# Kernel optimization log

Hardware: AMD Instinct MI355X
Metric: run time of the kernel (lower is better)

Reference implementation:

```python
import jax, jax.numpy as jnp
import numpy as np

N_NODES = 50000
N_EDGES = 800000
IN_DIM = 128
EDGE_DIM = 16
HIDDEN = 128
N_LAYERS = 3
N_GRAPHS = 256
BN_EPS = 1e-5


def setup_inputs() -> dict:
    key = jax.random.key(0)
    ks = jax.random.split(key, 24)
    s = 0.05
    inp = {
        "x": jax.random.normal(ks[0], (N_NODES, IN_DIM), jnp.float32),
        "edge_index": jax.random.randint(ks[1], (2, N_EDGES), 0, N_NODES, jnp.int32),
        "edge_attr": jax.random.normal(ks[2], (N_EDGES, EDGE_DIM), jnp.float32),
        "batch": jnp.sort(jax.random.randint(ks[3], (N_NODES,), 0, N_GRAPHS, jnp.int32)),
        "n_graphs": N_GRAPHS,
        # input projection
        "lin_in_w": jax.random.normal(ks[4], (IN_DIM, HIDDEN), jnp.float32) * s,
        "lin_in_b": jnp.zeros((HIDDEN,), jnp.float32),
        # per-layer message MLP (stacked over layers)
        "msg_w1": jax.random.normal(ks[5], (N_LAYERS, HIDDEN + EDGE_DIM, HIDDEN), jnp.float32) * s,
        "msg_b1": jnp.zeros((N_LAYERS, HIDDEN), jnp.float32),
        "msg_w2": jax.random.normal(ks[6], (N_LAYERS, HIDDEN, HIDDEN), jnp.float32) * s,
        "msg_b2": jnp.zeros((N_LAYERS, HIDDEN), jnp.float32),
        # BatchNorm (eval mode: running stats)
        "bn_gamma": jnp.ones((N_LAYERS, HIDDEN), jnp.float32),
        "bn_beta": jnp.zeros((N_LAYERS, HIDDEN), jnp.float32),
        "bn_mean": jax.random.normal(ks[7], (N_LAYERS, HIDDEN), jnp.float32) * 0.01,
        "bn_var": jax.random.uniform(ks[8], (N_LAYERS, HIDDEN), jnp.float32, 0.5, 1.5),
        # GRUCell params (PyTorch layout: [3*H, H], gate order r,z,n)
        "gru_wih": jax.random.normal(ks[9], (N_LAYERS, 3 * HIDDEN, HIDDEN), jnp.float32) * s,
        "gru_whh": jax.random.normal(ks[10], (N_LAYERS, 3 * HIDDEN, HIDDEN), jnp.float32) * s,
        "gru_bih": jnp.zeros((N_LAYERS, 3 * HIDDEN), jnp.float32),
        "gru_bhh": jnp.zeros((N_LAYERS, 3 * HIDDEN), jnp.float32),
        # readout linear: [2H -> H]
        "ro_w": jax.random.normal(ks[11], (2 * HIDDEN, HIDDEN), jnp.float32) * s,
        "ro_b": jnp.zeros((HIDDEN,), jnp.float32),
    }
    return inp


def _gru_cell(x, h, wih, whh, bih, bhh):
    gi = x @ wih.T + bih  # [N, 3H]
    gh = h @ whh.T + bhh
    ir, iz, inn = jnp.split(gi, 3, axis=1)
    hr, hz, hn = jnp.split(gh, 3, axis=1)
    r = jax.nn.sigmoid(ir + hr)
    z = jax.nn.sigmoid(iz + hz)
    n = jnp.tanh(inn + r * hn)
    return (1.0 - z) * n + z * h


def reference(x, edge_index, edge_attr, batch, n_graphs,
              lin_in_w, lin_in_b, msg_w1, msg_b1, msg_w2, msg_b2,
              bn_gamma, bn_beta, bn_mean, bn_var,
              gru_wih, gru_whh, gru_bih, gru_bhh, ro_w, ro_b):
    h = jax.nn.relu(x @ lin_in_w + lin_in_b)  # [N, H]
    src, dst = edge_index[0], edge_index[1]
    n_nodes = h.shape[0]
    for l in range(N_LAYERS):
        m_in = jnp.concatenate([h[src], edge_attr], axis=1)  # [E, H+Ed]
        m = jax.nn.relu(m_in @ msg_w1[l] + msg_b1[l]) @ msg_w2[l] + msg_b2[l]  # [E, H]
        agg = jax.ops.segment_sum(m, dst, num_segments=n_nodes)  # scatter-add
        h_new = _gru_cell(agg, h, gru_wih[l], gru_whh[l], gru_bih[l], gru_bhh[l])
        bn = (h_new - bn_mean[l]) * jax.lax.rsqrt(bn_var[l] + BN_EPS) * bn_gamma[l] + bn_beta[l]
        h = h + bn  # dropout is identity in eval mode
    # readout: segment mean + segment max over graphs
    cnt = jax.ops.segment_sum(jnp.ones((n_nodes, 1), h.dtype), batch, num_segments=n_graphs)
    z_sum = jax.ops.segment_sum(h, batch, num_segments=n_graphs)
    z_mean = z_sum / jnp.maximum(cnt, 1.0)
    z_max = jax.ops.segment_max(h, batch, num_segments=n_graphs)
    z_max = jnp.where(cnt > 0, z_max, 0.0)  # empty graphs -> 0 (as in torch code)
    z = jax.nn.relu(jnp.concatenate([z_mean, z_max], axis=1) @ ro_w + ro_b)
    return z
```

## Files before the change

kernel.cpp:

```cpp
#include <hip/hip_runtime.h>
#include <math.h>

constexpr int NN = 50000;
constexpr int NE = 800000;
constexpr int H  = 128;
constexpr int ED = 16;
constexpr int NL = 3;
constexpr int NG = 256;

typedef __attribute__((ext_vector_type(8))) short bf8;
typedef __attribute__((ext_vector_type(4))) float f32x4;

__device__ __forceinline__ unsigned short f2bf(float f) {
    unsigned u = __float_as_uint(f);
    unsigned r = (u + 0x7FFFu + ((u >> 16) & 1u)) >> 16;
    return (unsigned short)r;
}
__device__ __forceinline__ float bf2f(unsigned short b) {
    return __uint_as_float(((unsigned)b) << 16);
}

__global__ __launch_bounds__(256) void k_zero4(float4* __restrict__ a, int n4) {
    int i = blockIdx.x * 256 + threadIdx.x;
    if (i < n4) a[i] = make_float4(0.f, 0.f, 0.f, 0.f);
}

__global__ __launch_bounds__(256) void k_sort_zero(int* __restrict__ counts) {
    int i = blockIdx.x * 256 + threadIdx.x;
    counts[i] = 0;
}

__global__ __launch_bounds__(256) void k_hist(const int* __restrict__ ei,
                                              int* __restrict__ counts) {
    int e = blockIdx.x * 256 + threadIdx.x;
    if (e < NE) atomicAdd(&counts[ei[NE + e]], 1);
}

__global__ __launch_bounds__(256) void k_scan1(const int* __restrict__ counts,
                                               int* __restrict__ incl,
                                               int* __restrict__ bsum) {
    __shared__ int s[256];
    int t = threadIdx.x;
    int i = blockIdx.x * 256 + t;
    int v = counts[i];
    s[t] = v;
    __syncthreads();
    #pragma unroll
    for (int off = 1; off < 256; off <<= 1) {
        int x = (t >= off) ? s[t - off] : 0;
        __syncthreads();
        s[t] += x;
        __syncthreads();
    }
    incl[i] = s[t];
    if (t == 255) bsum[blockIdx.x] = s[255];
}

__global__ __launch_bounds__(256) void k_scan2(int* __restrict__ bsum) {
    __shared__ int s[256];
    int t = threadIdx.x;
    int v = (t < 196) ? bsum[t] : 0;
    s[t] = v;
    __syncthreads();
    #pragma unroll
    for (int off = 1; off < 256; off <<= 1) {
        int x = (t >= off) ? s[t - off] : 0;
        __syncthreads();
        s[t] += x;
        __syncthreads();
    }
    if (t < 196) bsum[t] = s[t] - v;
}

__global__ __launch_bounds__(256) void k_scan3(const int* __restrict__ counts,
                                               const int* __restrict__ incl,
                                               const int* __restrict__ bsum,
                                               int* __restrict__ cur) {
    int i = blockIdx.x * 256 + threadIdx.x;
    cur[i] = incl[i] - counts[i] + bsum[blockIdx.x];
}

__global__ __launch_bounds__(256) void k_scatter_perm(const int* __restrict__ ei,
                                                      int* __restrict__ cur,
                                                      int* __restrict__ perm) {
    int e = blockIdx.x * 256 + threadIdx.x;
    if (e < NE) {
        int d = ei[NE + e];
        int pos = atomicAdd(&cur[d], 1);
        perm[pos] = e;
    }
}

__global__ __launch_bounds__(256) void k_gather(const int* __restrict__ ei,
                                                const float* __restrict__ ea,
                                                int* __restrict__ perm,
                                                int* __restrict__ dsts,
                                                unsigned short* __restrict__ ea_bf) {
    int i = blockIdx.x * 256 + threadIdx.x;
    if (i >= NE) return;
    int e = perm[i];
    perm[i] = ei[e];
    dsts[i] = ei[NE + e];
    const float4* s = (const float4*)(ea + (size_t)e * ED);
    float4 v[4];
    #pragma unroll
    for (int j = 0; j < 4; ++j) v[j] = s[j];
    union { uint4 u[2]; unsigned short sh[16]; } pk;
    #pragma unroll
    for (int j = 0; j < 4; ++j) {
        pk.sh[j * 4 + 0] = f2bf(v[j].x); pk.sh[j * 4 + 1] = f2bf(v[j].y);
        pk.sh[j * 4 + 2] = f2bf(v[j].z); pk.sh[j * 4 + 3] = f2bf(v[j].w);
    }
    uint4* d = (uint4*)(ea_bf + (size_t)i * 16);
    d[0] = pk.u[0];
    d[1] = pk.u[1];
}

__global__ __launch_bounds__(256) void k_prep(const float* __restrict__ wih,
                                              const float* __restrict__ whh,
                                              const float* __restrict__ w1,
                                              const float* __restrict__ w2,
                                              const float* __restrict__ lin_w,
                                              unsigned short* __restrict__ wgru,
                                              unsigned short* __restrict__ w1et,
                                              unsigned short* __restrict__ w2t,
                                              unsigned short* __restrict__ w1ht,
                                              unsigned short* __restrict__ winT) {
    int i = blockIdx.x * 256 + threadIdx.x;
    if (i < 294912) {
        int m = i / 147456, rem = i % 147456;
        wgru[i] = f2bf((m == 0 ? wih : whh)[rem]);
        return;
    }
    i -= 294912;
    if (i < NL * 128 * 32) {
        int l = i / 4096, rem = i % 4096;
        int n = rem >> 5, k = rem & 31;
        float v = (k < ED) ? w1[(size_t)l * 144 * 128 + (size_t)(128 + k) * 128 + n] : 0.f;
        w1et[i] = f2bf(v);
        return;
    }
    i -= NL * 128 * 32;
    if (i < NL * 128 * 128) {
        int l = i / 16384, rem = i % 16384;
        int n = rem >> 7, k = rem & 127;
        w2t[i] = f2bf(w2[(size_t)l * 16384 + (size_t)k * 128 + n]);
        return;
    }
    i -= NL * 128 * 128;
    if (i < NL * 128 * 128) {
        int l = i / 16384, rem = i % 16384;
        int n = rem >> 7, k = rem & 127;
        w1ht[i] = f2bf(w1[(size_t)l * 144 * 128 + (size_t)k * 128 + n]);
        return;
    }
    i -= NL * 128 * 128;
    if (i < 128 * 128) {
        int n = i >> 7, k = i & 127;
        winT[i] = f2bf(lin_w[k * 128 + n]);
    }
}

__global__ __launch_bounds__(256) void k_inproj(const float* __restrict__ x,
                                                const unsigned short* __restrict__ winT,
                                                const float* __restrict__ bias,
                                                const unsigned short* __restrict__ w1h0,
                                                float* __restrict__ h,
                                                unsigned short* __restrict__ p_bf) {
    __shared__ unsigned short As[32][136];
    const int t = threadIdx.x;
    const int w = t >> 6, lane = t & 63, l15 = lane & 15, q = lane >> 4;
    const int n0 = blockIdx.x * 32;

    bf8 bfr[2][4];
    #pragma unroll
    for (int nt = 0; nt < 2; ++nt) {
        int n = w * 32 + nt * 16 + l15;
        #pragma unroll
        for (int ks = 0; ks < 4; ++ks)
            bfr[nt][ks] = *(const bf8*)(winT + (size_t)n * 128 + ks * 32 + q * 8);
    }

    {
        int r = t >> 3, cs = (t & 7) * 16;
        int row = n0 + r;
        float4 v[4];
        if (row < NN) {
            const float4* src = (const float4*)(x + (size_t)row * H + cs);
            #pragma unroll
            for (int j = 0; j < 4; ++j) v[j] = src[j];
        } else {
            #pragma unroll
            for (int j = 0; j < 4; ++j) v[j] = make_float4(0.f, 0.f, 0.f, 0.f);
        }
        union { uint4 u[2]; unsigned short s[16]; } pk;
        #pragma unroll
        for (int j = 0; j < 4; ++j) {
            pk.s[j * 4 + 0] = f2bf(v[j].x); pk.s[j * 4 + 1] = f2bf(v[j].y);
            pk.s[j * 4 + 2] = f2bf(v[j].z); pk.s[j * 4 + 3] = f2bf(v[j].w);
        }
        *(uint4*)&As[r][cs] = pk.u[0];
        *(uint4*)&As[r][cs + 8] = pk.u[1];
    }
    __syncthreads();

    f32x4 acc[2][2];
    #pragma unroll
    for (int mt = 0; mt < 2; ++mt)
        #pragma unroll
        for (int nt = 0; nt < 2; ++nt) acc[mt][nt] = {0.f, 0.f, 0.f, 0.f};

    #pragma unroll
    for (int ks = 0; ks < 4; ++ks) {
        #pragma unroll
        for (int mt = 0; mt < 2; ++mt) {
            bf8 af = *(const bf8*)&As[mt * 16 + l15][ks * 32 + q * 8];
            acc[mt][0] = __builtin_amdgcn_mfma_f32_16x16x32_bf16(af, bfr[0][ks], acc[mt][0], 0, 0, 0);
            acc[mt][1] = __builtin_amdgcn_mfma_f32_16x16x32_bf16(af, bfr[1][ks], acc[mt][1], 0, 0, 0);
        }
    }
    __syncthreads();

    #pragma unroll
    for (int nt = 0; nt < 2; ++nt) {
        int col = w * 32 + nt * 16 + l15;
        float bv = bias[col];
        #pragma unroll
        for (int mt = 0; mt < 2; ++mt) {
            #pragma unroll
            for (int r = 0; r < 4; ++r) {
                int nl = mt * 16 + q * 4 + r;
                int node = n0 + nl;
                float v = fmaxf(acc[mt][nt][r] + bv, 0.f);
                if (node < NN) h[(size_t)node * H + col] = v;
                As[nl][col] = f2bf(v);
            }
        }
    }
    __syncthreads();

    bf8 pfr[2][4];
    #pragma unroll
    for (int nt = 0; nt < 2; ++nt) {
        int n = w * 32 + nt * 16 + l15;
        #pragma unroll
        for (int ks = 0; ks < 4; ++ks)
            pfr[nt][ks] = *(const bf8*)(w1h0 + (size_t)n * 128 + ks * 32 + q * 8);
    }
    f32x4 accp[2][2];
    #pragma unroll
    for (int mt = 0; mt < 2; ++mt)
        #pragma unroll
        for (int nt = 0; nt < 2; ++nt) accp[mt][nt] = {0.f, 0.f, 0.f, 0.f};
    #pragma unroll
    for (int ks = 0; ks < 4; ++ks) {
        #pragma unroll
        for (int mt = 0; mt < 2; ++mt) {
            bf8 af = *(const bf8*)&As[mt * 16 + l15][ks * 32 + q * 8];
            accp[mt][0] = __builtin_amdgcn_mfma_f32_16x16x32_bf16(af, pfr[0][ks], accp[mt][0], 0, 0, 0);
            accp[mt][1] = __builtin_amdgcn_mfma_f32_16x16x32_bf16(af, pfr[1][ks], accp[mt][1], 0, 0, 0);
        }
    }
    #pragma unroll
    for (int nt = 0; nt < 2; ++nt) {
        int col = w * 32 + nt * 16 + l15;
        #pragma unroll
        for (int mt = 0; mt < 2; ++mt) {
            #pragma unroll
            for (int r = 0; r < 4; ++r) {
                int node = n0 + mt * 16 + q * 4 + r;
                if (node < NN) p_bf[(size_t)node * H + col] = f2bf(accp[mt][nt][r]);
            }
        }
    }
}

__global__ __launch_bounds__(256, 4) void k_edge_mfma(
        const unsigned short* __restrict__ p,
        const int* __restrict__ srcs,
        const int* __restrict__ dsts,
        const unsigned short* __restrict__ ea_bf,
        const unsigned short* __restrict__ w1et,
        const float* __restrict__ b1,
        const unsigned short* __restrict__ w2t,
        const float* __restrict__ b2,
        float* __restrict__ agg) {
    __shared__ unsigned short u_s[64][136];
    __shared__ int src_s[64], dst_s[64];

    const int t    = threadIdx.x;
    const int w    = t >> 6;
    const int lane = t & 63;
    const int l15  = lane & 15;
    const int q    = lane >> 4;

    bf8 w1f[2];
    bf8 w2f[2][4];
    float b1v[2], b2v[2];
    #pragma unroll
    for (int nt = 0; nt < 2; ++nt) {
        int n = w * 32 + nt * 16 + l15;
        w1f[nt] = *(const bf8*)(w1et + (size_t)n * 32 + q * 8);
        #pragma unroll
        for (int ks = 0; ks < 4; ++ks)
            w2f[nt][ks] = *(const bf8*)(w2t + (size_t)n * 128 + ks * 32 + q * 8);
        b1v[nt] = b1[n];
        b2v[nt] = b2[n];
    }

    const f32x4 zero = {0.f, 0.f, 0.f, 0.f};

    for (int base = blockIdx.x * 64; base < NE; base += gridDim.x * 64) {
        if (t < 64)       src_s[t] = srcs[base + t];
        else if (t < 128) dst_s[t - 64] = dsts[base + t - 64];
        __syncthreads();

        {
            int row = t >> 4, seg = t & 15;
            #pragma unroll
            for (int it = 0; it < 4; ++it) {
                int rr = row + 16 * it;
                *(uint4*)&u_s[rr][seg * 8] =
                    *(const uint4*)(p + (size_t)src_s[rr] * H + seg * 8);
            }
        }

        f32x4 acc1[4][2];
        #pragma unroll
        for (int mt = 0; mt < 4; ++mt) {
            bf8 af = {0, 0, 0, 0, 0, 0, 0, 0};
            if (q < 2)
                af = *(const bf8*)(ea_bf + (size_t)(base + mt * 16 + l15) * 16 + q * 8);
            #pragma unroll
            for (int nt = 0; nt < 2; ++nt)
                acc1[mt][nt] = __builtin_amdgcn_mfma_f32_16x16x32_bf16(af, w1f[nt], zero, 0, 0, 0);
        }
        __syncthreads();

        #pragma unroll
        for (int mt = 0; mt < 4; ++mt) {
            #pragma unroll
            for (int r = 0; r < 4; ++r) {
                int er = mt * 16 + q * 4 + r;
                #pragma unroll
                for (int nt = 0; nt < 2; ++nt) {
                    int col = w * 32 + nt * 16 + l15;
                    float v = acc1[mt][nt][r] + bf2f(u_s[er][col]) + b1v[nt];
                    u_s[er][col] = f2bf(fmaxf(v, 0.f));
                }
            }
        }
        __syncthreads();

        f32x4 acc2[4][2];
        #pragma unroll
        for (int mt = 0; mt < 4; ++mt)
            #pragma unroll
            for (int nt = 0; nt < 2; ++nt) acc2[mt][nt] = zero;

        #pragma unroll
        for (int ks = 0; ks < 4; ++ks) {
            #pragma unroll
            for (int mt = 0; mt < 4; ++mt) {
                bf8 af = *(const bf8*)&u_s[mt * 16 + l15][ks * 32 + q * 8];
                acc2[mt][0] = __builtin_amdgcn_mfma_f32_16x16x32_bf16(af, w2f[0][ks], acc2[mt][0], 0, 0, 0);
                acc2[mt][1] = __builtin_amdgcn_mfma_f32_16x16x32_bf16(af, w2f[1][ks], acc2[mt][1], 0, 0, 0);
            }
        }
        __syncthreads();

        #pragma unroll
        for (int mt = 0; mt < 4; ++mt) {
            #pragma unroll
            for (int r = 0; r < 4; ++r) {
                int er = mt * 16 + q * 4 + r;
                #pragma unroll
                for (int nt = 0; nt < 2; ++nt) {
                    int col = w * 32 + nt * 16 + l15;
                    u_s[er][col] = f2bf(acc2[mt][nt][r] + b2v[nt]);
                }
            }
        }
        __syncthreads();

        {
            int c = t & 127, hh = t >> 7;
            float sum = 0.f;
            int prev = dst_s[hh * 32];
            #pragma unroll 4
            for (int i = 0; i < 32; ++i) {
                int e = hh * 32 + i;
                int d = dst_s[e];
                float v = bf2f(u_s[e][c]);
                if (d != prev) {
                    atomicAdd(&agg[(size_t)prev * H + c], sum);
                    sum = 0.f;
                    prev = d;
                }
                sum += v;
            }
            atomicAdd(&agg[(size_t)prev * H + c], sum);
        }
        __syncthreads();
    }
}

__device__ __forceinline__ float sigmoidf_(float x) { return 1.f / (1.f + expf(-x)); }

__global__ __launch_bounds__(256) void k_gru_mfma(const float* __restrict__ agg,
                                                  float* __restrict__ h,
                                                  const unsigned short* __restrict__ wih,
                                                  const unsigned short* __restrict__ whh,
                                                  const float* __restrict__ bih,
                                                  const float* __restrict__ bhh,
                                                  const float* __restrict__ gamma,
                                                  const float* __restrict__ beta,
                                                  const float* __restrict__ mean,
                                                  const float* __restrict__ var,
                                                  const unsigned short* __restrict__ w1h_next,
                                                  unsigned short* __restrict__ p_bf) {
    __shared__ unsigned short ab[32][136];
    __shared__ unsigned short hb[32][136];
    __shared__ float hf[32][132];
    const int t = threadIdx.x;
    const int w = t >> 6, lane = t & 63, l15 = lane & 15, q = lane >> 4;
    const int n0 = blockIdx.x * 32;

    {
        int r = t >> 3, cs = (t & 7) * 16;
        int row = n0 + r;
        float4 va[4], vh[4];
        if (row < NN) {
            const float4* sa = (const float4*)(agg + (size_t)row * H + cs);
            const float4* sh = (const float4*)(h + (size_t)row * H + cs);
            #pragma unroll
            for (int j = 0; j < 4; ++j) { va[j] = sa[j]; vh[j] = sh[j]; }
        } else {
            #pragma unroll
            for (int j = 0; j < 4; ++j) {
                va[j] = make_float4(0.f, 0.f, 0.f, 0.f);
                vh[j] = va[j];
            }
        }
        union { uint4 u[2]; unsigned short s[16]; } pa, ph;
        #pragma unroll
        for (int j = 0; j < 4; ++j) {
            pa.s[j * 4 + 0] = f2bf(va[j].x); pa.s[j * 4 + 1] = f2bf(va[j].y);
            pa.s[j * 4 + 2] = f2bf(va[j].z); pa.s[j * 4 + 3] = f2bf(va[j].w);
            ph.s[j * 4 + 0] = f2bf(vh[j].x); ph.s[j * 4 + 1] = f2bf(vh[j].y);
            ph.s[j * 4 + 2] = f2bf(vh[j].z); ph.s[j * 4 + 3] = f2bf(vh[j].w);
            *(float4*)&hf[r][cs + j * 4] = vh[j];
        }
        *(uint4*)&ab[r][cs] = pa.u[0];  *(uint4*)&ab[r][cs + 8] = pa.u[1];
        *(uint4*)&hb[r][cs] = ph.u[0];  *(uint4*)&hb[r][cs + 8] = ph.u[1];
    }
    __syncthreads();

    f32x4 acc[2][2][3][2];
    #pragma unroll
    for (int mt = 0; mt < 2; ++mt)
        #pragma unroll
        for (int io = 0; io < 2; ++io)
            #pragma unroll
            for (int g = 0; g < 3; ++g)
                #pragma unroll
                for (int nt = 0; nt < 2; ++nt) acc[mt][io][g][nt] = {0.f, 0.f, 0.f, 0.f};

    #pragma unroll
    for (int ks = 0; ks < 4; ++ks) {
        bf8 a_a[2], a_h[2];
        #pragma unroll
        for (int mt = 0; mt < 2; ++mt) {
            a_a[mt] = *(const bf8*)&ab[mt * 16 + l15][ks * 32 + q * 8];
            a_h[mt] = *(const bf8*)&hb[mt * 16 + l15][ks * 32 + q * 8];
        }
        #pragma unroll
        for (int g = 0; g < 3; ++g) {
            #pragma unroll
            for (int nt = 0; nt < 2; ++nt) {
                int n = g * 128 + w * 32 + nt * 16 + l15;
                bf8 bi = *(const bf8*)(wih + (size_t)n * 128 + ks * 32 + q * 8);
                bf8 bh = *(const bf8*)(whh + (size_t)n * 128 + ks * 32 + q * 8);
                #pragma unroll
                for (int mt = 0; mt < 2; ++mt) {
                    acc[mt][0][g][nt] = __builtin_amdgcn_mfma_f32_16x16x32_bf16(a_a[mt], bi, acc[mt][0][g][nt], 0, 0, 0);
                    acc[mt][1][g][nt] = __builtin_amdgcn_mfma_f32_16x16x32_bf16(a_h[mt], bh, acc[mt][1][g][nt], 0, 0, 0);
                }
            }
        }
    }

    float rout[2][2][4];
    #pragma unroll
    for (int nt = 0; nt < 2; ++nt) {
        int col = w * 32 + nt * 16 + l15;
        float bir = bih[col], biz = bih[128 + col], bin = bih[256 + col];
        float bhr = bhh[col], bhz = bhh[128 + col], bhn = bhh[256 + col];
        float ga = gamma[col], be = beta[col], mu = mean[col];
        float iv = rsqrtf(var[col] + 1e-5f);
        #pragma unroll
        for (int mt = 0; mt < 2; ++mt) {
            #pragma unroll
            for (int r = 0; r < 4; ++r) {
                int nl = mt * 16 + q * 4 + r;
                int node = n0 + nl;
                float ir = acc[mt][0][0][nt][r] + bir;
                float iz = acc[mt][0][1][nt][r] + biz;
                float in = acc[mt][0][2][nt][r] + bin;
                float hr = acc[mt][1][0][nt][r] + bhr;
                float hz = acc[mt][1][1][nt][r] + bhz;
                float hn = acc[mt][1][2][nt][r] + bhn;
                float rg = sigmoidf_(ir + hr);
                float zg = sigmoidf_(iz + hz);
                float ng = tanhf(in + rg * hn);
                float hv = hf[nl][col];
                float hnew = (1.f - zg) * ng + zg * hv;
                float bn = (hnew - mu) * iv * ga + be;
                float out = hv + bn;
                rout[nt][mt][r] = out;
                if (node < NN) h[(size_t)node * H + col] = out;
            }
        }
    }

    if (w1h_next != nullptr) {
        __syncthreads();
        #pragma unroll
        for (int nt = 0; nt < 2; ++nt) {
            int col = w * 32 + nt * 16 + l15;
            #pragma unroll
            for (int mt = 0; mt < 2; ++mt)
                #pragma unroll
                for (int r = 0; r < 4; ++r)
                    hb[mt * 16 + q * 4 + r][col] = f2bf(rout[nt][mt][r]);
        }
        __syncthreads();

        f32x4 accp[2][2];
        #pragma unroll
        for (int mt = 0; mt < 2; ++mt)
            #pragma unroll
            for (int nt = 0; nt < 2; ++nt) accp[mt][nt] = {0.f, 0.f, 0.f, 0.f};
        #pragma unroll
        for (int ks = 0; ks < 4; ++ks) {
            bf8 pf0, pf1;
            {
                int n = w * 32 + l15;
                pf0 = *(const bf8*)(w1h_next + (size_t)n * 128 + ks * 32 + q * 8);
                pf1 = *(const bf8*)(w1h_next + (size_t)(n + 16) * 128 + ks * 32 + q * 8);
            }
            #pragma unroll
            for (int mt = 0; mt < 2; ++mt) {
                bf8 af = *(const bf8*)&hb[mt * 16 + l15][ks * 32 + q * 8];
                accp[mt][0] = __builtin_amdgcn_mfma_f32_16x16x32_bf16(af, pf0, accp[mt][0], 0, 0, 0);
                accp[mt][1] = __builtin_amdgcn_mfma_f32_16x16x32_bf16(af, pf1, accp[mt][1], 0, 0, 0);
            }
        }
        #pragma unroll
        for (int nt = 0; nt < 2; ++nt) {
            int col = w * 32 + nt * 16 + l15;
            #pragma unroll
            for (int mt = 0; mt < 2; ++mt) {
                #pragma unroll
                for (int r = 0; r < 4; ++r) {
                    int node = n0 + mt * 16 + q * 4 + r;
                    if (node < NN) p_bf[(size_t)node * H + col] = f2bf(accp[mt][nt][r]);
                }
            }
        }
    }
}

__device__ __forceinline__ unsigned fkey(float f) {
    unsigned b = __float_as_uint(f);
    return (b & 0x80000000u) ? ~b : (b | 0x80000000u);
}
__device__ __forceinline__ float funkey(unsigned k) {
    unsigned b = (k & 0x80000000u) ? (k & 0x7FFFFFFFu) : ~k;
    return __uint_as_float(b);
}

__global__ __launch_bounds__(256) void k_ro_init(float* __restrict__ gsum,
                                                 unsigned* __restrict__ gmaxb,
                                                 float* __restrict__ gcnt) {
    int i = blockIdx.x * 256 + threadIdx.x;
    if (i < NG * H) { gsum[i] = 0.f; gmaxb[i] = 0u; }
    if (i < NG) gcnt[i] = 0.f;
}

__global__ __launch_bounds__(256) void k_ro_scan(const float* __restrict__ h,
                                                 const int* __restrict__ batch,
                                                 float* __restrict__ gsum,
                                                 unsigned* __restrict__ gmaxb,
                                                 float* __restrict__ gcnt) {
    __shared__ int bt_s[64];
    const int t = threadIdx.x;
    const int n0 = blockIdx.x * 64;
    if (t < 64) bt_s[t] = (n0 + t < NN) ? batch[n0 + t] : -1;
    __syncthreads();

    int c = t & 127, hh = t >> 7;
    float sum = 0.f, mx = -3.4e38f, cnt = 0.f;
    int prev = bt_s[hh * 32];
    #pragma unroll 4
    for (int i = 0; i < 32; ++i) {
        int e = hh * 32 + i;
        int g = bt_s[e];
        if (g != prev) {
            if (prev >= 0) {
                atomicAdd(&gsum[prev * H + c], sum);
                atomicMax(&gmaxb[prev * H + c], fkey(mx));
                if (c == 0) atomicAdd(&gcnt[prev], cnt);
            }
            sum = 0.f; mx = -3.4e38f; cnt = 0.f;
            prev = g;
        }
        if (g >= 0) {
            float v = h[(size_t)(n0 + e) * H + c];
            sum += v;
            mx = fmaxf(mx, v);
            cnt += 1.f;
        }
    }
    if (prev >= 0) {
        atomicAdd(&gsum[prev * H + c], sum);
        atomicMax(&gmaxb[prev * H + c], fkey(mx));
        if (c == 0) atomicAdd(&gcnt[prev], cnt);
    }
}

__global__ __launch_bounds__(128) void k_ro_final(const float* __restrict__ gsum,
                                                  const unsigned* __restrict__ gmaxb,
                                                  const float* __restrict__ gcnt,
                                                  const float* __restrict__ row,
                                                  const float* __restrict__ rob,
                                                  float* __restrict__ out) {
    __shared__ float cat[256];
    const int g = blockIdx.x, t = threadIdx.x;
    float cnt = gcnt[g];
    float inv = 1.f / fmaxf(cnt, 1.f);
    cat[t] = gsum[g * H + t] * inv;
    float mx = funkey(gmaxb[g * H + t]);
    cat[128 + t] = (cnt > 0.f) ? mx : 0.f;
    __syncthreads();
    float acc = rob[t];
    #pragma unroll 4
    for (int k = 0; k < 256; ++k) acc += cat[k] * row[k * H + t];
    out[g * H + t] = fmaxf(acc, 0.f);
}

extern "C" void kernel_launch(void* const* d_in, const int* in_sizes, int n_in,
                              void* d_out, int out_size, void* d_ws, size_t ws_size,
                              hipStream_t stream) {
    const float* x        = (const float*)d_in[0];
    const int*   ei       = (const int*)d_in[1];
    const float* ea       = (const float*)d_in[2];
    const int*   batch    = (const int*)d_in[3];
    const float* lin_in_w = (const float*)d_in[5];
    const float* lin_in_b = (const float*)d_in[6];
    const float* msg_w1   = (const float*)d_in[7];
    const float* msg_b1   = (const float*)d_in[8];
    const float* msg_w2   = (const float*)d_in[9];
    const float* msg_b2   = (const float*)d_in[10];
    const float* bn_gamma = (const float*)d_in[11];
    const float* bn_beta  = (const float*)d_in[12];
    const float* bn_mean  = (const float*)d_in[13];
    const float* bn_var   = (const float*)d_in[14];
    const float* gru_wih  = (const float*)d_in[15];
    const float* gru_whh  = (const float*)d_in[16];
    const float* gru_bih  = (const float*)d_in[17];
    const float* gru_bhh  = (const float*)d_in[18];
    const float* ro_w     = (const float*)d_in[19];
    const float* ro_b     = (const float*)d_in[20];

    float* ws = (float*)d_ws;
    float*          h     = ws;
    float*          agg   = ws + 6400000;
    unsigned short* p_bf  = (unsigned short*)(ws + 12800000);
    float*          gsum  = ws + 16000000;
    unsigned*       gmaxb = (unsigned*)(ws + 16032768);
    float*          gcnt  = ws + 16065536;
    unsigned short* wgru  = (unsigned short*)(ws + 16065792);
    unsigned short* w1et  = (unsigned short*)(ws + 16213248);
    unsigned short* w2t   = (unsigned short*)(ws + 16219392);
    unsigned short* w1ht  = (unsigned short*)(ws + 16243968);
    unsigned short* winT  = (unsigned short*)(ws + 16268544);
    int*            cnts  = (int*)(ws + 16276736);
    int*            incl  = (int*)(ws + 16326912);
    int*            cur   = (int*)(ws + 16377088);
    int*            bsum  = (int*)(ws + 16427264);
    int*            srcs  = (int*)(ws + 16427520);
    int*            dsts  = (int*)(ws + 17227520);
    unsigned short* ea_bf = (unsigned short*)(ws + 18027520);

    k_prep<<<1648, 256, 0, stream>>>(gru_wih, gru_whh, msg_w1, msg_w2, lin_in_w,
                                     wgru, w1et, w2t, w1ht, winT);

    k_sort_zero<<<196, 256, 0, stream>>>(cnts);
    k_hist<<<3125, 256, 0, stream>>>(ei, cnts);
    k_scan1<<<196, 256, 0, stream>>>(cnts, incl, bsum);
    k_scan2<<<1, 256, 0, stream>>>(bsum);
    k_scan3<<<196, 256, 0, stream>>>(cnts, incl, bsum, cur);
    k_scatter_perm<<<3125, 256, 0, stream>>>(ei, cur, srcs);
    k_gather<<<3125, 256, 0, stream>>>(ei, ea, srcs, dsts, ea_bf);

    k_inproj<<<1563, 256, 0, stream>>>(x, winT, lin_in_b, w1ht, h, p_bf);

    for (int l = 0; l < NL; ++l) {
        k_zero4<<<6250, 256, 0, stream>>>((float4*)agg, 1600000);
        k_edge_mfma<<<1024, 256, 0, stream>>>(p_bf, srcs, dsts, ea_bf,
                                              w1et + (size_t)l * 4096, msg_b1 + l * 128,
                                              w2t + (size_t)l * 16384, msg_b2 + l * 128,
                                              agg);
        const unsigned short* w1h_next = (l + 1 < NL) ? (w1ht + (size_t)(l + 1) * 16384) : nullptr;
        k_gru_mfma<<<1563, 256, 0, stream>>>(agg, h,
                                             wgru + (size_t)l * 49152,
                                             wgru + (size_t)(NL + l) * 49152,
                                             gru_bih + l * 384, gru_bhh + l * 384,
                                             bn_gamma + l * 128, bn_beta + l * 128,
                                             bn_mean + l * 128, bn_var + l * 128,
                                             w1h_next, p_bf);
    }

    k_ro_init<<<128, 256, 0, stream>>>(gsum, gmaxb, gcnt);
    k_ro_scan<<<782, 256, 0, stream>>>(h, batch, gsum, gmaxb, gcnt);
    k_ro_final<<<NG, 128, 0, stream>>>(gsum, gmaxb, gcnt, ro_w, ro_b, (float*)d_out);
}
```

Before: 849.6 us.

## Fuse preprocessing into cooperative kernel, fold zeroing into compute kernels, enlarge edge tile

Replaces the chain of preprocessing kernels (weight prep, histogram, three scans, permutation scatter, gather) with a single cooperative kernel that uses grid-wide syncs. The separate agg and readout zeroing kernels are removed: agg is zeroed inside the input projection and GRU kernels, and the readout accumulators are zeroed in the last GRU launch. The edge kernel tile grows from 64 to 128 edges, processed in two halves, and the GRU activations switch to fast exp-based sigmoid and tanh. The aim is fewer launches and less zeroing traffic. The trade-offs are grid-sync overhead, a 256-block cooperative grid doing strided work, more shared memory per edge block, and slightly different numerics.

```diff
diff --git a/kernel.cpp b/kernel.cpp
--- a/kernel.cpp
+++ b/kernel.cpp
@@ -1,5 +1,8 @@
 #include <hip/hip_runtime.h>
+#include <hip/hip_cooperative_groups.h>
 #include <math.h>
+
+namespace cg = cooperative_groups;
 
 constexpr int NN = 50000;
 constexpr int NE = 800000;
@@ -7,6 +10,9 @@
 constexpr int ED = 16;
 constexpr int NL = 3;
 constexpr int NG = 256;
+constexpr int NBINS = 50176;
+constexpr int TE = 128;
+constexpr int PREP_TOTAL = 294912 + NL*128*32 + NL*128*128 + NL*128*128 + 128*128;
 
 typedef __attribute__((ext_vector_type(8))) short bf8;
 typedef __attribute__((ext_vector_type(4))) float f32x4;
@@ -19,114 +25,22 @@
 __device__ __forceinline__ float bf2f(unsigned short b) {
     return __uint_as_float(((unsigned)b) << 16);
 }
-
-__global__ __launch_bounds__(256) void k_zero4(float4* __restrict__ a, int n4) {
-    int i = blockIdx.x * 256 + threadIdx.x;
-    if (i < n4) a[i] = make_float4(0.f, 0.f, 0.f, 0.f);
-}
-
-__global__ __launch_bounds__(256) void k_sort_zero(int* __restrict__ counts) {
-    int i = blockIdx.x * 256 + threadIdx.x;
-    counts[i] = 0;
-}
-
-__global__ __launch_bounds__(256) void k_hist(const int* __restrict__ ei,
-                                              int* __restrict__ counts) {
-    int e = blockIdx.x * 256 + threadIdx.x;
-    if (e < NE) atomicAdd(&counts[ei[NE + e]], 1);
-}
-
-__global__ __launch_bounds__(256) void k_scan1(const int* __restrict__ counts,
-                                               int* __restrict__ incl,
-                                               int* __restrict__ bsum) {
-    __shared__ int s[256];
-    int t = threadIdx.x;
-    int i = blockIdx.x * 256 + t;
-    int v = counts[i];
-    s[t] = v;
-    __syncthreads();
-    #pragma unroll
-    for (int off = 1; off < 256; off <<= 1) {
-        int x = (t >= off) ? s[t - off] : 0;
-        __syncthreads();
-        s[t] += x;
-        __syncthreads();
-    }
-    incl[i] = s[t];
-    if (t == 255) bsum[blockIdx.x] = s[255];
-}
-
-__global__ __launch_bounds__(256) void k_scan2(int* __restrict__ bsum) {
-    __shared__ int s[256];
-    int t = threadIdx.x;
-    int v = (t < 196) ? bsum[t] : 0;
-    s[t] = v;
-    __syncthreads();
-    #pragma unroll
-    for (int off = 1; off < 256; off <<= 1) {
-        int x = (t >= off) ? s[t - off] : 0;
-        __syncthreads();
-        s[t] += x;
-        __syncthreads();
-    }
-    if (t < 196) bsum[t] = s[t] - v;
-}
-
-__global__ __launch_bounds__(256) void k_scan3(const int* __restrict__ counts,
-                                               const int* __restrict__ incl,
-                                               const int* __restrict__ bsum,
-                                               int* __restrict__ cur) {
-    int i = blockIdx.x * 256 + threadIdx.x;
-    cur[i] = incl[i] - counts[i] + bsum[blockIdx.x];
-}
-
-__global__ __launch_bounds__(256) void k_scatter_perm(const int* __restrict__ ei,
-                                                      int* __restrict__ cur,
-                                                      int* __restrict__ perm) {
-    int e = blockIdx.x * 256 + threadIdx.x;
-    if (e < NE) {
-        int d = ei[NE + e];
-        int pos = atomicAdd(&cur[d], 1);
-        perm[pos] = e;
-    }
-}
-
-__global__ __launch_bounds__(256) void k_gather(const int* __restrict__ ei,
-                                                const float* __restrict__ ea,
-                                                int* __restrict__ perm,
-                                                int* __restrict__ dsts,
-                                                unsigned short* __restrict__ ea_bf) {
-    int i = blockIdx.x * 256 + threadIdx.x;
-    if (i >= NE) return;
-    int e = perm[i];
-    perm[i] = ei[e];
-    dsts[i] = ei[NE + e];
-    const float4* s = (const float4*)(ea + (size_t)e * ED);
-    float4 v[4];
-    #pragma unroll
-    for (int j = 0; j < 4; ++j) v[j] = s[j];
-    union { uint4 u[2]; unsigned short sh[16]; } pk;
-    #pragma unroll
-    for (int j = 0; j < 4; ++j) {
-        pk.sh[j * 4 + 0] = f2bf(v[j].x); pk.sh[j * 4 + 1] = f2bf(v[j].y);
-        pk.sh[j * 4 + 2] = f2bf(v[j].z); pk.sh[j * 4 + 3] = f2bf(v[j].w);
-    }
-    uint4* d = (uint4*)(ea_bf + (size_t)i * 16);
-    d[0] = pk.u[0];
-    d[1] = pk.u[1];
-}
-
-__global__ __launch_bounds__(256) void k_prep(const float* __restrict__ wih,
-                                              const float* __restrict__ whh,
-                                              const float* __restrict__ w1,
-                                              const float* __restrict__ w2,
-                                              const float* __restrict__ lin_w,
-                                              unsigned short* __restrict__ wgru,
-                                              unsigned short* __restrict__ w1et,
-                                              unsigned short* __restrict__ w2t,
-                                              unsigned short* __restrict__ w1ht,
-                                              unsigned short* __restrict__ winT) {
-    int i = blockIdx.x * 256 + threadIdx.x;
+__device__ __forceinline__ float fsig(float x) {
+    float e = __expf(fminf(-x, 80.f));
+    return 1.f / (1.f + e);
+}
+__device__ __forceinline__ float ftanh_(float x) {
+    float e = __expf(fminf(-2.f * x, 80.f));
+    return (1.f - e) / (1.f + e);
+}
+
+__device__ __forceinline__ void prep_one(int i,
+        const float* __restrict__ wih, const float* __restrict__ whh,
+        const float* __restrict__ w1, const float* __restrict__ w2,
+        const float* __restrict__ lin_w,
+        unsigned short* __restrict__ wgru, unsigned short* __restrict__ w1et,
+        unsigned short* __restrict__ w2t, unsigned short* __restrict__ w1ht,
+        unsigned short* __restrict__ winT) {
     if (i < 294912) {
         int m = i / 147456, rem = i % 147456;
         wgru[i] = f2bf((m == 0 ? wih : whh)[rem]);
@@ -161,12 +75,96 @@
     }
 }
 
+__global__ __launch_bounds__(256) void k_coop(
+        const float* __restrict__ wih, const float* __restrict__ whh,
+        const float* __restrict__ w1, const float* __restrict__ w2,
+        const float* __restrict__ lin_w,
+        unsigned short* __restrict__ wgru, unsigned short* __restrict__ w1et,
+        unsigned short* __restrict__ w2t, unsigned short* __restrict__ w1ht,
+        unsigned short* __restrict__ winT,
+        const int* __restrict__ ei, const float* __restrict__ ea,
+        int* __restrict__ cnts, int* __restrict__ incl, int* __restrict__ bsum,
+        int* __restrict__ cur, int* __restrict__ srcs, int* __restrict__ dsts,
+        unsigned short* __restrict__ ea_bf) {
+    cg::grid_group grid = cg::this_grid();
+    const int t = threadIdx.x;
+    const int gid = blockIdx.x * 256 + t;
+    const int GT = gridDim.x * 256;
+    __shared__ int s[256];
+
+    if (gid < NBINS) cnts[gid] = 0;
+    for (int i = gid; i < PREP_TOTAL; i += GT)
+        prep_one(i, wih, whh, w1, w2, lin_w, wgru, w1et, w2t, w1ht, winT);
+    grid.sync();
+
+    for (int e = gid; e < NE; e += GT) atomicAdd(&cnts[ei[NE + e]], 1);
+    grid.sync();
+
+    if (blockIdx.x < 196) {
+        int v = cnts[gid];
+        s[t] = v;
+        __syncthreads();
+        #pragma unroll
+        for (int off = 1; off < 256; off <<= 1) {
+            int x2 = (t >= off) ? s[t - off] : 0;
+            __syncthreads();
+            s[t] += x2;
+            __syncthreads();
+        }
+        incl[gid] = s[t];
+        if (t == 255) bsum[blockIdx.x] = s[255];
+    }
+    grid.sync();
+
+    if (blockIdx.x == 0) {
+        int v = (t < 196) ? bsum[t] : 0;
+        s[t] = v;
+        __syncthreads();
+        #pragma unroll
+        for (int off = 1; off < 256; off <<= 1) {
+            int x2 = (t >= off) ? s[t - off] : 0;
+            __syncthreads();
+            s[t] += x2;
+            __syncthreads();
+        }
+        if (t < 196) bsum[t] = s[t] - v;
+    }
+    grid.sync();
+
+    if (gid < NBINS) cur[gid] = incl[gid] - cnts[gid] + bsum[gid >> 8];
+    grid.sync();
+
+    for (int e = gid; e < NE; e += GT) {
+        int d = ei[NE + e];
+        int pos = atomicAdd(&cur[d], 1);
+        srcs[pos] = e;
+    }
+    grid.sync();
+
+    for (int i = gid; i < NE; i += GT) {
+        int e = srcs[i];
+        srcs[i] = ei[e];
+        dsts[i] = ei[NE + e];
+        const float4* sp = (const float4*)(ea + (size_t)e * ED);
+        float4 v0 = sp[0], v1 = sp[1], v2 = sp[2], v3 = sp[3];
+        union { uint4 u[2]; unsigned short sh[16]; } pk;
+        pk.sh[0] = f2bf(v0.x); pk.sh[1] = f2bf(v0.y); pk.sh[2] = f2bf(v0.z); pk.sh[3] = f2bf(v0.w);
+        pk.sh[4] = f2bf(v1.x); pk.sh[5] = f2bf(v1.y); pk.sh[6] = f2bf(v1.z); pk.sh[7] = f2bf(v1.w);
+        pk.sh[8] = f2bf(v2.x); pk.sh[9] = f2bf(v2.y); pk.sh[10] = f2bf(v2.z); pk.sh[11] = f2bf(v2.w);
+        pk.sh[12] = f2bf(v3.x); pk.sh[13] = f2bf(v3.y); pk.sh[14] = f2bf(v3.z); pk.sh[15] = f2bf(v3.w);
+        uint4* d4 = (uint4*)(ea_bf + (size_t)i * 16);
+        d4[0] = pk.u[0];
+        d4[1] = pk.u[1];
+    }
+}
+
 __global__ __launch_bounds__(256) void k_inproj(const float* __restrict__ x,
                                                 const unsigned short* __restrict__ winT,
                                                 const float* __restrict__ bias,
                                                 const unsigned short* __restrict__ w1h0,
                                                 float* __restrict__ h,
-                                                unsigned short* __restrict__ p_bf) {
+                                                unsigned short* __restrict__ p_bf,
+                                                float* __restrict__ agg) {
     __shared__ unsigned short As[32][136];
     const int t = threadIdx.x;
     const int w = t >> 6, lane = t & 63, l15 = lane & 15, q = lane >> 4;
@@ -203,6 +201,16 @@
         *(uint4*)&As[r][cs + 8] = pk.u[1];
     }
     __syncthreads();
+
+    {
+        int r = t >> 3, cs = (t & 7) * 16;
+        int row = n0 + r;
+        if (row < NN) {
+            float4 z = make_float4(0.f, 0.f, 0.f, 0.f);
+            float4* dz = (float4*)(agg + (size_t)row * H + cs);
+            dz[0] = z; dz[1] = z; dz[2] = z; dz[3] = z;
+        }
+    }
 
     f32x4 acc[2][2];
     #pragma unroll
@@ -285,8 +293,8 @@
         const unsigned short* __restrict__ w2t,
         const float* __restrict__ b2,
         float* __restrict__ agg) {
-    __shared__ unsigned short u_s[64][136];
-    __shared__ int src_s[64], dst_s[64];
+    __shared__ unsigned short u_s[TE][136];
+    __shared__ int src_s[TE], dst_s[TE];
 
     const int t    = threadIdx.x;
     const int w    = t >> 6;
@@ -310,74 +318,78 @@
 
     const f32x4 zero = {0.f, 0.f, 0.f, 0.f};
 
-    for (int base = blockIdx.x * 64; base < NE; base += gridDim.x * 64) {
-        if (t < 64)       src_s[t] = srcs[base + t];
-        else if (t < 128) dst_s[t - 64] = dsts[base + t - 64];
+    for (int base = blockIdx.x * TE; base < NE; base += gridDim.x * TE) {
+        if (t < TE) src_s[t] = srcs[base + t];
+        else        dst_s[t - TE] = dsts[base + t - TE];
         __syncthreads();
 
         {
             int row = t >> 4, seg = t & 15;
             #pragma unroll
-            for (int it = 0; it < 4; ++it) {
+            for (int it = 0; it < 8; ++it) {
                 int rr = row + 16 * it;
                 *(uint4*)&u_s[rr][seg * 8] =
                     *(const uint4*)(p + (size_t)src_s[rr] * H + seg * 8);
             }
         }
 
-        f32x4 acc1[4][2];
-        #pragma unroll
-        for (int mt = 0; mt < 4; ++mt) {
-            bf8 af = {0, 0, 0, 0, 0, 0, 0, 0};
-            if (q < 2)
-                af = *(const bf8*)(ea_bf + (size_t)(base + mt * 16 + l15) * 16 + q * 8);
-            #pragma unroll
-            for (int nt = 0; nt < 2; ++nt)
-                acc1[mt][nt] = __builtin_amdgcn_mfma_f32_16x16x32_bf16(af, w1f[nt], zero, 0, 0, 0);
+        #pragma unroll
+        for (int half = 0; half < 2; ++half) {
+            f32x4 acc1[4][2];
+            #pragma unroll
+            for (int m4 = 0; m4 < 4; ++m4) {
+                int mt = half * 4 + m4;
+                bf8 af = {0, 0, 0, 0, 0, 0, 0, 0};
+                if (q < 2)
+                    af = *(const bf8*)(ea_bf + (size_t)(base + mt * 16 + l15) * 16 + q * 8);
+                acc1[m4][0] = __builtin_amdgcn_mfma_f32_16x16x32_bf16(af, w1f[0], zero, 0, 0, 0);
+                acc1[m4][1] = __builtin_amdgcn_mfma_f32_16x16x32_bf16(af, w1f[1], zero, 0, 0, 0);
+            }
+            if (half == 0) __syncthreads();
+            #pragma unroll
+            for (int m4 = 0; m4 < 4; ++m4) {
+                #pragma unroll
+                for (int r = 0; r < 4; ++r) {
+                    int er = (half * 4 + m4) * 16 + q * 4 + r;
+                    #pragma unroll
+                    for (int nt = 0; nt < 2; ++nt) {
+                        int col = w * 32 + nt * 16 + l15;
+                        float v = acc1[m4][nt][r] + bf2f(u_s[er][col]) + b1v[nt];
+                        u_s[er][col] = f2bf(fmaxf(v, 0.f));
+                    }
+                }
+            }
         }
         __syncthreads();
 
         #pragma unroll
-        for (int mt = 0; mt < 4; ++mt) {
-            #pragma unroll
-            for (int r = 0; r < 4; ++r) {
-                int er = mt * 16 + q * 4 + r;
+        for (int half = 0; half < 2; ++half) {
+            f32x4 acc2[4][2];
+            #pragma unroll
+            for (int m4 = 0; m4 < 4; ++m4)
                 #pragma unroll
-                for (int nt = 0; nt < 2; ++nt) {
-                    int col = w * 32 + nt * 16 + l15;
-                    float v = acc1[mt][nt][r] + bf2f(u_s[er][col]) + b1v[nt];
-                    u_s[er][col] = f2bf(fmaxf(v, 0.f));
+                for (int nt = 0; nt < 2; ++nt) acc2[m4][nt] = zero;
+            #pragma unroll
+            for (int ks = 0; ks < 4; ++ks) {
+                #pragma unroll
+                for (int m4 = 0; m4 < 4; ++m4) {
+                    int mt = half * 4 + m4;
+                    bf8 af = *(const bf8*)&u_s[mt * 16 + l15][ks * 32 + q * 8];
+                    acc2[m4][0] = __builtin_amdgcn_mfma_f32_16x16x32_bf16(af, w2f[0][ks], acc2[m4][0], 0, 0, 0);
+                    acc2[m4][1] = __builtin_amdgcn_mfma_f32_16x16x32_bf16(af, w2f[1][ks], acc2[m4][1], 0, 0, 0);
                 }
             }
-        }
-        __syncthreads();
-
-        f32x4 acc2[4][2];
-        #pragma unroll
-        for (int mt = 0; mt < 4; ++mt)
-            #pragma unroll
-            for (int nt = 0; nt < 2; ++nt) acc2[mt][nt] = zero;
-
-        #pragma unroll
-        for (int ks = 0; ks < 4; ++ks) {
-            #pragma unroll
-            for (int mt = 0; mt < 4; ++mt) {
-                bf8 af = *(const bf8*)&u_s[mt * 16 + l15][ks * 32 + q * 8];
-                acc2[mt][0] = __builtin_amdgcn_mfma_f32_16x16x32_bf16(af, w2f[0][ks], acc2[mt][0], 0, 0, 0);
-                acc2[mt][1] = __builtin_amdgcn_mfma_f32_16x16x32_bf16(af, w2f[1][ks], acc2[mt][1], 0, 0, 0);
-            }
-        }
-        __syncthreads();
-
-        #pragma unroll
-        for (int mt = 0; mt < 4; ++mt) {
-            #pragma unroll
-            for (int r = 0; r < 4; ++r) {
-                int er = mt * 16 + q * 4 + r;
+            __syncthreads();
+            #pragma unroll
+            for (int m4 = 0; m4 < 4; ++m4) {
                 #pragma unroll
-                for (int nt = 0; nt < 2; ++nt) {
-                    int col = w * 32 + nt * 16 + l15;
-                    u_s[er][col] = f2bf(acc2[mt][nt][r] + b2v[nt]);
+                for (int r = 0; r < 4; ++r) {
+                    int er = (half * 4 + m4) * 16 + q * 4 + r;
+                    #pragma unroll
+                    for (int nt = 0; nt < 2; ++nt) {
+                        int col = w * 32 + nt * 16 + l15;
+                        u_s[er][col] = f2bf(acc2[m4][nt][r] + b2v[nt]);
+                    }
                 }
             }
         }
@@ -385,29 +397,28 @@
 
         {
             int c = t & 127, hh = t >> 7;
+            float* aggc = agg + c;
             float sum = 0.f;
-            int prev = dst_s[hh * 32];
+            int prev = dst_s[hh * 64];
             #pragma unroll 4
-            for (int i = 0; i < 32; ++i) {
-                int e = hh * 32 + i;
+            for (int i = 0; i < 64; ++i) {
+                int e = hh * 64 + i;
                 int d = dst_s[e];
                 float v = bf2f(u_s[e][c]);
                 if (d != prev) {
-                    atomicAdd(&agg[(size_t)prev * H + c], sum);
+                    atomicAdd(aggc + (size_t)prev * H, sum);
                     sum = 0.f;
                     prev = d;
                 }
                 sum += v;
             }
-            atomicAdd(&agg[(size_t)prev * H + c], sum);
+            atomicAdd(aggc + (size_t)prev * H, sum);
         }
         __syncthreads();
     }
 }
 
-__device__ __forceinline__ float sigmoidf_(float x) { return 1.f / (1.f + expf(-x)); }
-
-__global__ __launch_bounds__(256) void k_gru_mfma(const float* __restrict__ agg,
+__global__ __launch_bounds__(256) void k_gru_mfma(float* __restrict__ agg,
                                                   float* __restrict__ h,
                                                   const unsigned short* __restrict__ wih,
                                                   const unsigned short* __restrict__ whh,
@@ -418,7 +429,8 @@
                                                   const float* __restrict__ mean,
                                                   const float* __restrict__ var,
                                                   const unsigned short* __restrict__ w1h_next,
-                                                  unsigned short* __restrict__ p_bf) {
+                                                  unsigned short* __restrict__ p_bf,
+                                                  int* __restrict__ ro_z) {
     __shared__ unsigned short ab[32][136];
     __shared__ unsigned short hb[32][136];
     __shared__ float hf[32][132];
@@ -455,6 +467,17 @@
         *(uint4*)&hb[r][cs] = ph.u[0];  *(uint4*)&hb[r][cs + 8] = ph.u[1];
     }
     __syncthreads();
+
+    if (w1h_next != nullptr) {
+        int r = t >> 3, cs = (t & 7) * 16;
+        int row = n0 + r;
+        if (row < NN) {
+            float4 z = make_float4(0.f, 0.f, 0.f, 0.f);
+            float4* dz = (float4*)(agg + (size_t)row * H + cs);
+            dz[0] = z; dz[1] = z; dz[2] = z; dz[3] = z;
+        }
+    }
+    if (ro_z != nullptr && blockIdx.x < 257) ro_z[blockIdx.x * 256 + t] = 0;
 
     f32x4 acc[2][2][3][2];
     #pragma unroll
@@ -510,9 +533,9 @@
                 float hr = acc[mt][1][0][nt][r] + bhr;
                 float hz = acc[mt][1][1][nt][r] + bhz;
                 float hn = acc[mt][1][2][nt][r] + bhn;
-                float rg = sigmoidf_(ir + hr);
-                float zg = sigmoidf_(iz + hz);
-                float ng = tanhf(in + rg * hn);
+                float rg = fsig(ir + hr);
+                float zg = fsig(iz + hz);
+                float ng = ftanh_(in + rg * hn);
                 float hv = hf[nl][col];
                 float hnew = (1.f - zg) * ng + zg * hv;
                 float bn = (hnew - mu) * iv * ga + be;
@@ -578,14 +601,6 @@
 __device__ __forceinline__ float funkey(unsigned k) {
     unsigned b = (k & 0x80000000u) ? (k & 0x7FFFFFFFu) : ~k;
     return __uint_as_float(b);
-}
-
-__global__ __launch_bounds__(256) void k_ro_init(float* __restrict__ gsum,
-                                                 unsigned* __restrict__ gmaxb,
-                                                 float* __restrict__ gcnt) {
-    int i = blockIdx.x * 256 + threadIdx.x;
-    if (i < NG * H) { gsum[i] = 0.f; gmaxb[i] = 0u; }
-    if (i < NG) gcnt[i] = 0.f;
 }
 
 __global__ __launch_bounds__(256) void k_ro_scan(const float* __restrict__ h,
@@ -693,36 +708,36 @@
     int*            dsts  = (int*)(ws + 17227520);
     unsigned short* ea_bf = (unsigned short*)(ws + 18027520);
 
-    k_prep<<<1648, 256, 0, stream>>>(gru_wih, gru_whh, msg_w1, msg_w2, lin_in_w,
-                                     wgru, w1et, w2t, w1ht, winT);
-
-    k_sort_zero<<<196, 256, 0, stream>>>(cnts);
-    k_hist<<<3125, 256, 0, stream>>>(ei, cnts);
-    k_scan1<<<196, 256, 0, stream>>>(cnts, incl, bsum);
-    k_scan2<<<1, 256, 0, stream>>>(bsum);
-    k_scan3<<<196, 256, 0, stream>>>(cnts, incl, bsum, cur);
-    k_scatter_perm<<<3125, 256, 0, stream>>>(ei, cur, srcs);
-    k_gather<<<3125, 256, 0, stream>>>(ei, ea, srcs, dsts, ea_bf);
-
-    k_inproj<<<1563, 256, 0, stream>>>(x, winT, lin_in_b, w1ht, h, p_bf);
+    {
+        void* cargs[] = {
+            (void*)&gru_wih, (void*)&gru_whh, (void*)&msg_w1, (void*)&msg_w2,
+            (void*)&lin_in_w,
+            (void*)&wgru, (void*)&w1et, (void*)&w2t, (void*)&w1ht, (void*)&winT,
+            (void*)&ei, (void*)&ea,
+            (void*)&cnts, (void*)&incl, (void*)&bsum, (void*)&cur,
+            (void*)&srcs, (void*)&dsts, (void*)&ea_bf
+        };
+        hipLaunchCooperativeKernel((void*)k_coop, dim3(256), dim3(256), cargs, 0, stream);
+    }
+
+    k_inproj<<<1563, 256, 0, stream>>>(x, winT, lin_in_b, w1ht, h, p_bf, agg);
 
     for (int l = 0; l < NL; ++l) {
-        k_zero4<<<6250, 256, 0, stream>>>((float4*)agg, 1600000);
         k_edge_mfma<<<1024, 256, 0, stream>>>(p_bf, srcs, dsts, ea_bf,
                                               w1et + (size_t)l * 4096, msg_b1 + l * 128,
                                               w2t + (size_t)l * 16384, msg_b2 + l * 128,
                                               agg);
         const unsigned short* w1h_next = (l + 1 < NL) ? (w1ht + (size_t)(l + 1) * 16384) : nullptr;
+        int* ro_z = (l == NL - 1) ? (int*)gsum : nullptr;
         k_gru_mfma<<<1563, 256, 0, stream>>>(agg, h,
                                              wgru + (size_t)l * 49152,
                                              wgru + (size_t)(NL + l) * 49152,
                                              gru_bih + l * 384, gru_bhh + l * 384,
                                              bn_gamma + l * 128, bn_beta + l * 128,
                                              bn_mean + l * 128, bn_var + l * 128,
-                                             w1h_next, p_bf);
-    }
-
-    k_ro_init<<<128, 256, 0, stream>>>(gsum, gmaxb, gcnt);
+                                             w1h_next, p_bf, ro_z);
+    }
+
     k_ro_scan<<<782, 256, 0, stream>>>(h, batch, gsum, gmaxb, gcnt);
     k_ro_final<<<NG, 128, 0, stream>>>(gsum, gmaxb, gcnt, ro_w, ro_b, (float*)d_out);
 }
```

Result: slower. 0.9997 ms (+17.7%).
